# Optimization experiments

Hardware: AMD Instinct MI355X
Metric: run time of the kernel (lower is better)

The kernel has to match this reference:

```python
import jax, jax.numpy as jnp
import numpy as np

N_NODES = 100000


def setup_inputs() -> dict:
    key = jax.random.key(0)
    k1, k2, k3, k4, k5 = jax.random.split(key, 5)
    h = jax.random.normal(k1, (N_NODES, 128), dtype=jnp.float32)
    norm = jax.random.uniform(k2, (N_NODES, 1), dtype=jnp.float32)  # D^{-1/2}-style per-node norm
    W = jax.random.normal(k3, (128, 64), dtype=jnp.float32) * 0.05
    b = jnp.zeros((64,), dtype=jnp.float32)
    src = jax.random.randint(k4, (1600000,), 0, N_NODES, dtype=jnp.int32)
    dst = jax.random.randint(k5, (1600000,), 0, N_NODES, dtype=jnp.int32)
    return {"h": h, "norm": norm, "W": W, "b": b, "src": src, "dst": dst}


def reference(h, norm, W, b, src, dst):
    # Dense feature transform: g.ndata['h'] = h @ W   (dropout is identity at inference)
    hw = jnp.matmul(h, W)  # [N, out]
    # Message: src feature scaled by src norm
    msg = hw[src] * norm[src]  # [E, out]
    # Reduce: sum messages into dst, scale by dst norm
    agg = jax.ops.segment_sum(msg, dst, num_segments=N_NODES) * norm  # [N, out]
    out = agg + b
    return jax.nn.relu(out)
```

## Files before the change

kernel.cpp:

```cpp
#include <hip/hip_runtime.h>


typedef unsigned int u32;
typedef unsigned short u16;
typedef __attribute__((ext_vector_type(8))) short s16x8;
typedef __attribute__((ext_vector_type(4))) float f32x4;

#define NB_LOG 6
#define NPB 64
#define CAP 2048
#define MAXB 2048
#define EPB 8192
#define RT 256

__device__ __forceinline__ float bf2f(u16 v) {
  return __uint_as_float(((u32)v) << 16);
}
__device__ __forceinline__ u16 f2bf(float f) {
  u32 u = __float_as_uint(f);
  return (u16)((u + 0x7fffu + ((u >> 16) & 1u)) >> 16);
}
__device__ __forceinline__ void acc_bf16x4(float4& a, uint2 v) {
  a.x += __uint_as_float(v.x << 16);
  a.y += __uint_as_float(v.x & 0xFFFF0000u);
  a.z += __uint_as_float(v.y << 16);
  a.w += __uint_as_float(v.y & 0xFFFF0000u);
}

__global__ __launch_bounds__(256) void wconv(
    const float* __restrict__ W, u16* __restrict__ Wtg, u32* __restrict__ gcur) {
  int o = blockIdx.x * 256 + threadIdx.x;
  int j = o & 7, col = (o >> 3) & 15, kq = (o >> 7) & 3, ks = (o >> 9) & 3,
      ct = (o >> 11) & 3;
  int k = ks * 32 + kq * 8 + j;
  int n = ct * 16 + col;
  Wtg[o] = f2bf(W[k * 64 + n]);
  if (o < MAXB) gcur[o] = 0;
}

__global__ __launch_bounds__(256) void gemm_mfma(
    const float* __restrict__ h, const float* __restrict__ norm,
    const u16* __restrict__ Wtg, u16* __restrict__ scaledh, int N) {
  int lane = threadIdx.x & 63, wid = threadIdx.x >> 6;
  int col = lane & 15, kq = lane >> 4;

  s16x8 bfrag[4][4];
#pragma unroll
  for (int ct = 0; ct < 4; ++ct)
#pragma unroll
    for (int ks = 0; ks < 4; ++ks) {
      int f = ct * 16 + ks * 4 + kq;
      bfrag[ct][ks] =
          *reinterpret_cast<const s16x8*>(Wtg + ((size_t)(f * 16 + col) * 8));
    }

  int row0 = blockIdx.x * 64 + wid * 16;
  int myrow = row0 + col;
  int ldrow = myrow < N ? myrow : (N - 1);
  const float* __restrict__ hrow = h + (size_t)ldrow * 128 + kq * 8;

  f32x4 acc[4];
#pragma unroll
  for (int ct = 0; ct < 4; ++ct) acc[ct] = (f32x4){0.f, 0.f, 0.f, 0.f};

#pragma unroll
  for (int ks = 0; ks < 4; ++ks) {
    float4 x0 = *reinterpret_cast<const float4*>(hrow + ks * 32);
    float4 x1 = *reinterpret_cast<const float4*>(hrow + ks * 32 + 4);
    s16x8 a;
    a[0] = (short)f2bf(x0.x); a[1] = (short)f2bf(x0.y);
    a[2] = (short)f2bf(x0.z); a[3] = (short)f2bf(x0.w);
    a[4] = (short)f2bf(x1.x); a[5] = (short)f2bf(x1.y);
    a[6] = (short)f2bf(x1.z); a[7] = (short)f2bf(x1.w);
#pragma unroll
    for (int ct = 0; ct < 4; ++ct)
      acc[ct] =
          __builtin_amdgcn_mfma_f32_16x16x32_bf16(a, bfrag[ct][ks], acc[ct], 0, 0, 0);
  }

#pragma unroll
  for (int reg = 0; reg < 4; ++reg) {
    int node = row0 + kq * 4 + reg;
    if (node < N) {
      float nm = norm[node];
#pragma unroll
      for (int ct = 0; ct < 4; ++ct)
        scaledh[(size_t)node * 64 + ct * 16 + col] = f2bf(acc[ct][reg] * nm);
    }
  }
}

__global__ __launch_bounds__(1024) void bin_edges(
    const int* __restrict__ src, const int* __restrict__ dst,
    u32* __restrict__ gcur, u32* __restrict__ bins, int E) {
  __shared__ u32 lhist[MAXB];
  __shared__ u32 lbase[MAXB];
  int t = threadIdx.x;
  for (int i = t; i < MAXB; i += 1024) lhist[i] = 0;
  __syncthreads();
  int e0 = blockIdx.x * EPB;
  int s[8], d[8];
  u32 r[8];
#pragma unroll
  for (int k = 0; k < 8; ++k) {
    int e = e0 + k * 1024 + t;
    bool ok = e < E;
    s[k] = ok ? src[e] : 0;
    d[k] = ok ? dst[e] : -1;
  }
#pragma unroll
  for (int k = 0; k < 8; ++k) {
    if (d[k] >= 0) r[k] = atomicAdd(&lhist[d[k] >> NB_LOG], 1u);
  }
  __syncthreads();
  for (int i = t; i < MAXB; i += 1024) {
    u32 c = lhist[i];
    lbase[i] = c ? atomicAdd(&gcur[i], c) : 0u;
  }
  __syncthreads();
#pragma unroll
  for (int k = 0; k < 8; ++k) {
    if (d[k] >= 0) {
      int bk = d[k] >> NB_LOG;
      u32 p = lbase[bk] + r[k];
      if (p < CAP)
        bins[(size_t)bk * CAP + p] = ((u32)s[k] << NB_LOG) | (u32)(d[k] & (NPB - 1));
    }
  }
}

__global__ __launch_bounds__(RT) void bucket_reduce(
    const u16* __restrict__ scaledh, const u32* __restrict__ bins,
    const u32* __restrict__ gcur, const float* __restrict__ norm,
    const float4* __restrict__ bias4, float* __restrict__ out, int N) {
  __shared__ u32 hist[NPB];
  __shared__ u32 startp[NPB + 1];
  __shared__ u32 sorted[CAP];
  int bkt = blockIdx.x;
  int t = threadIdx.x, lane = t & 63, wid = t >> 6;
  int cnt = (int)gcur[bkt];
  if (cnt > CAP) cnt = CAP;
  if (t < NPB) hist[t] = 0;
  __syncthreads();

  const u32* __restrict__ my = bins + (size_t)bkt * CAP;
  u32 w[CAP / RT];
  u32 rk[CAP / RT];
#pragma unroll
  for (int k = 0; k < CAP / RT; ++k) {
    int e = k * RT + t;
    w[k] = (e < cnt) ? my[e] : 0xFFFFFFFFu;
  }
#pragma unroll
  for (int k = 0; k < CAP / RT; ++k) {
    if (w[k] != 0xFFFFFFFFu)
      rk[k] = atomicAdd(&hist[w[k] & (NPB - 1)], 1u);
  }
  __syncthreads();
  if (t < NPB) {
    u32 v = hist[t];
    u32 inc = v;
#pragma unroll
    for (int m = 1; m < NPB; m <<= 1) {
      u32 x = __shfl_up(inc, m);
      if (t >= m) inc += x;
    }
    startp[t] = inc - v;
    if (t == NPB - 1) startp[NPB] = inc;
  }
  __syncthreads();
#pragma unroll
  for (int k = 0; k < CAP / RT; ++k) {
    if (w[k] != 0xFFFFFFFFu)
      sorted[startp[w[k] & (NPB - 1)] + rk[k]] = w[k] >> NB_LOG;
  }
  __syncthreads();

  int grp = lane >> 4, c4 = lane & 15;
  float4 bl = bias4[c4];
  int base = bkt << NB_LOG;
  int cm1 = cnt - 1;
  const u16* __restrict__ sh = scaledh + (c4 << 2);
#pragma unroll
  for (int round = 0; round < 2; ++round) {
    int rA = (wid << 4) + (round << 3) + grp;
    int rB = rA + 4;
    int jA = (int)startp[rA], eA = (int)startp[rA + 1];
    int jB = (int)startp[rB], eB = (int)startp[rB + 1];
    float4 aA0 = make_float4(0.f, 0.f, 0.f, 0.f);
    float4 aA1 = make_float4(0.f, 0.f, 0.f, 0.f);
    float4 aB0 = make_float4(0.f, 0.f, 0.f, 0.f);
    float4 aB1 = make_float4(0.f, 0.f, 0.f, 0.f);
    while (jA < eA || jB < eB) {
      int iA0 = (int)sorted[min(jA + 0, cm1)];
      int iA1 = (int)sorted[min(jA + 1, cm1)];
      int iA2 = (int)sorted[min(jA + 2, cm1)];
      int iA3 = (int)sorted[min(jA + 3, cm1)];
      int iB0 = (int)sorted[min(jB + 0, cm1)];
      int iB1 = (int)sorted[min(jB + 1, cm1)];
      int iB2 = (int)sorted[min(jB + 2, cm1)];
      int iB3 = (int)sorted[min(jB + 3, cm1)];
      uint2 vA0 = *reinterpret_cast<const uint2*>(sh + ((size_t)iA0 << 6));
      uint2 vA1 = *reinterpret_cast<const uint2*>(sh + ((size_t)iA1 << 6));
      uint2 vA2 = *reinterpret_cast<const uint2*>(sh + ((size_t)iA2 << 6));
      uint2 vA3 = *reinterpret_cast<const uint2*>(sh + ((size_t)iA3 << 6));
      uint2 vB0 = *reinterpret_cast<const uint2*>(sh + ((size_t)iB0 << 6));
      uint2 vB1 = *reinterpret_cast<const uint2*>(sh + ((size_t)iB1 << 6));
      uint2 vB2 = *reinterpret_cast<const uint2*>(sh + ((size_t)iB2 << 6));
      uint2 vB3 = *reinterpret_cast<const uint2*>(sh + ((size_t)iB3 << 6));
      uint2 z = make_uint2(0u, 0u);
      vA0 = (jA + 0 < eA) ? vA0 : z;
      vA1 = (jA + 1 < eA) ? vA1 : z;
      vA2 = (jA + 2 < eA) ? vA2 : z;
      vA3 = (jA + 3 < eA) ? vA3 : z;
      vB0 = (jB + 0 < eB) ? vB0 : z;
      vB1 = (jB + 1 < eB) ? vB1 : z;
      vB2 = (jB + 2 < eB) ? vB2 : z;
      vB3 = (jB + 3 < eB) ? vB3 : z;
      acc_bf16x4(aA0, vA0);
      acc_bf16x4(aA1, vA1);
      acc_bf16x4(aA0, vA2);
      acc_bf16x4(aA1, vA3);
      acc_bf16x4(aB0, vB0);
      acc_bf16x4(aB1, vB1);
      acc_bf16x4(aB0, vB2);
      acc_bf16x4(aB1, vB3);
      jA += 4;
      jB += 4;
    }
    int nodeA = base + rA, nodeB = base + rB;
    if (nodeA < N) {
      float nm = norm[nodeA];
      float4 o;
      o.x = fmaxf(fmaf(aA0.x + aA1.x, nm, bl.x), 0.f);
      o.y = fmaxf(fmaf(aA0.y + aA1.y, nm, bl.y), 0.f);
      o.z = fmaxf(fmaf(aA0.z + aA1.z, nm, bl.z), 0.f);
      o.w = fmaxf(fmaf(aA0.w + aA1.w, nm, bl.w), 0.f);
      *reinterpret_cast<float4*>(out + (size_t)nodeA * 64 + (c4 << 2)) = o;
    }
    if (nodeB < N) {
      float nm = norm[nodeB];
      float4 o;
      o.x = fmaxf(fmaf(aB0.x + aB1.x, nm, bl.x), 0.f);
      o.y = fmaxf(fmaf(aB0.y + aB1.y, nm, bl.y), 0.f);
      o.z = fmaxf(fmaf(aB0.z + aB1.z, nm, bl.z), 0.f);
      o.w = fmaxf(fmaf(aB0.w + aB1.w, nm, bl.w), 0.f);
      *reinterpret_cast<float4*>(out + (size_t)nodeB * 64 + (c4 << 2)) = o;
    }
  }
}

__global__ __launch_bounds__(256) void zero_out(float4* __restrict__ o4, size_t n4) {
  size_t tid = blockIdx.x * 256 + threadIdx.x;
  size_t stride = (size_t)gridDim.x * 256;
  for (size_t i = tid; i < n4; i += stride) o4[i] = make_float4(0.f, 0.f, 0.f, 0.f);
}

__global__ __launch_bounds__(256) void scatter_edges(
    const u16* __restrict__ scaledh, const int* __restrict__ src,
    const int* __restrict__ dst, float* __restrict__ agg, int E) {
  int lane = threadIdx.x & 63;
  int gwid = (blockIdx.x * 256 + threadIdx.x) >> 6;
  int nw = (gridDim.x * 256) >> 6;
  for (int e = gwid; e < E; e += nw) {
    int s = __builtin_amdgcn_readfirstlane(src[e]);
    int d = __builtin_amdgcn_readfirstlane(dst[e]);
    float v = bf2f(scaledh[(size_t)s * 64 + lane]);
    unsafeAtomicAdd(&agg[(size_t)d * 64 + lane], v);
  }
}

__global__ __launch_bounds__(256) void finalize(
    float4* __restrict__ out4, const float* __restrict__ norm,
    const float4* __restrict__ b4, int N) {
  size_t total4 = (size_t)N * 16;
  size_t tid = blockIdx.x * 256 + threadIdx.x;
  size_t stride = (size_t)gridDim.x * 256;
  for (size_t t = tid; t < total4; t += stride) {
    int i = (int)(t >> 4), q = (int)(t & 15);
    float4 v = out4[t];
    float nm = norm[i];
    float4 bb = b4[q];
    v.x = fmaxf(fmaf(v.x, nm, bb.x), 0.f);
    v.y = fmaxf(fmaf(v.y, nm, bb.y), 0.f);
    v.z = fmaxf(fmaf(v.z, nm, bb.z), 0.f);
    v.w = fmaxf(fmaf(v.w, nm, bb.w), 0.f);
    out4[t] = v;
  }
}

extern "C" void kernel_launch(void* const* d_in, const int* in_sizes, int n_in,
                              void* d_out, int out_size, void* d_ws, size_t ws_size,
                              hipStream_t stream) {
  const float* h    = (const float*)d_in[0];
  const float* norm = (const float*)d_in[1];
  const float* W    = (const float*)d_in[2];
  const float* b    = (const float*)d_in[3];
  const int*   src  = (const int*)d_in[4];
  const int*   dst  = (const int*)d_in[5];

  int N = in_sizes[1];
  int E = in_sizes[4];
  int nbuckets = (N + NPB - 1) >> NB_LOG;
  int nrb = (N + 63) >> 6;
  int nbinb = (E + EPB - 1) / EPB;

  char* ws = (char*)d_ws;
  size_t off = 0;
  u16* scaledh = (u16*)(ws + off); off += (((size_t)N * 64 * 2) + 255) & ~(size_t)255;
  u32* gcur    = (u32*)(ws + off); off += (MAXB * 4 + 255) & ~(size_t)255;
  u16* Wtg     = (u16*)(ws + off); off += (8192 * 2 + 255) & ~(size_t)255;
  u32* bins    = (u32*)(ws + off); off += (size_t)MAXB * CAP * 4;
  size_t needed = off;
  size_t needed_fb = (size_t)((char*)bins - ws);

  if (ws_size >= needed && nbuckets <= MAXB) {
    wconv<<<32, 256, 0, stream>>>(W, Wtg, gcur);
    gemm_mfma<<<nrb, 256, 0, stream>>>(h, norm, Wtg, scaledh, N);
    bin_edges<<<nbinb, 1024, 0, stream>>>(src, dst, gcur, bins, E);
    bucket_reduce<<<nbuckets, RT, 0, stream>>>(scaledh, bins, gcur, norm,
                                               (const float4*)b, (float*)d_out, N);
  } else if (ws_size >= needed_fb) {
    float* agg = (float*)d_out;
    wconv<<<32, 256, 0, stream>>>(W, Wtg, gcur);
    gemm_mfma<<<nrb, 256, 0, stream>>>(h, norm, Wtg, scaledh, N);
    zero_out<<<1024, 256, 0, stream>>>((float4*)agg, (size_t)N * 16);
    scatter_edges<<<2048, 256, 0, stream>>>(scaledh, src, dst, agg, E);
    finalize<<<1024, 256, 0, stream>>>((float4*)agg, norm, (const float4*)b, N);
  }
}
```

Baseline: 79.12 us.

## Merge edge binning and MFMA GEMM into one launch with role-split blocks

The separate gemm_mfma and bin_edges launches are merged into one kernel. The first nbinb blocks bin edges and the remaining blocks each run the bf16 MFMA transform on 256 rows, using 16 waves of 1024 threads. The two independent stages can now run concurrently on the GPU, and one launch and its inter-kernel gap are removed. In exchange, GEMM blocks reserve the 16KB of shared memory the binning path needs and run at 1024 threads, which may lower occupancy. The original GEMM kernel is kept unchanged as a fallback variant.

```diff
diff --git a/kernel.cpp b/kernel.cpp
--- a/kernel.cpp
+++ b/kernel.cpp
@@ -12,6 +12,7 @@
 #define MAXB 2048
 #define EPB 8192
 #define RT 256
+#define GROWS 256
 
 __device__ __forceinline__ float bf2f(u16 v) {
   return __uint_as_float(((u32)v) << 16);
@@ -38,9 +39,50 @@
   if (o < MAXB) gcur[o] = 0;
 }
 
-__global__ __launch_bounds__(256) void gemm_mfma(
+__global__ __launch_bounds__(1024) void bin_and_gemm(
     const float* __restrict__ h, const float* __restrict__ norm,
-    const u16* __restrict__ Wtg, u16* __restrict__ scaledh, int N) {
+    const u16* __restrict__ Wtg, u16* __restrict__ scaledh, int N, int nbinb,
+    const int* __restrict__ src, const int* __restrict__ dst,
+    u32* __restrict__ gcur, u32* __restrict__ bins, int E) {
+  __shared__ u32 lhist[MAXB];
+  __shared__ u32 lbase[MAXB];
+
+  if ((int)blockIdx.x < nbinb) {
+    int t = threadIdx.x;
+    for (int i = t; i < MAXB; i += 1024) lhist[i] = 0;
+    __syncthreads();
+    int e0 = blockIdx.x * EPB;
+    int s[8], d[8];
+    u32 r[8];
+#pragma unroll
+    for (int k = 0; k < 8; ++k) {
+      int e = e0 + k * 1024 + t;
+      bool ok = e < E;
+      s[k] = ok ? src[e] : 0;
+      d[k] = ok ? dst[e] : -1;
+    }
+#pragma unroll
+    for (int k = 0; k < 8; ++k) {
+      if (d[k] >= 0) r[k] = atomicAdd(&lhist[d[k] >> NB_LOG], 1u);
+    }
+    __syncthreads();
+    for (int i = t; i < MAXB; i += 1024) {
+      u32 c = lhist[i];
+      lbase[i] = c ? atomicAdd(&gcur[i], c) : 0u;
+    }
+    __syncthreads();
+#pragma unroll
+    for (int k = 0; k < 8; ++k) {
+      if (d[k] >= 0) {
+        int bk = d[k] >> NB_LOG;
+        u32 p = lbase[bk] + r[k];
+        if (p < CAP)
+          bins[(size_t)bk * CAP + p] = ((u32)s[k] << NB_LOG) | (u32)(d[k] & (NPB - 1));
+      }
+    }
+    return;
+  }
+
   int lane = threadIdx.x & 63, wid = threadIdx.x >> 6;
   int col = lane & 15, kq = lane >> 4;
 
@@ -54,7 +96,7 @@
           *reinterpret_cast<const s16x8*>(Wtg + ((size_t)(f * 16 + col) * 8));
     }
 
-  int row0 = blockIdx.x * 64 + wid * 16;
+  int row0 = ((int)blockIdx.x - nbinb) * GROWS + wid * 16;
   int myrow = row0 + col;
   int ldrow = myrow < N ? myrow : (N - 1);
   const float* __restrict__ hrow = h + (size_t)ldrow * 128 + kq * 8;
@@ -86,45 +128,6 @@
 #pragma unroll
       for (int ct = 0; ct < 4; ++ct)
         scaledh[(size_t)node * 64 + ct * 16 + col] = f2bf(acc[ct][reg] * nm);
-    }
-  }
-}
-
-__global__ __launch_bounds__(1024) void bin_edges(
-    const int* __restrict__ src, const int* __restrict__ dst,
-    u32* __restrict__ gcur, u32* __restrict__ bins, int E) {
-  __shared__ u32 lhist[MAXB];
-  __shared__ u32 lbase[MAXB];
-  int t = threadIdx.x;
-  for (int i = t; i < MAXB; i += 1024) lhist[i] = 0;
-  __syncthreads();
-  int e0 = blockIdx.x * EPB;
-  int s[8], d[8];
-  u32 r[8];
-#pragma unroll
-  for (int k = 0; k < 8; ++k) {
-    int e = e0 + k * 1024 + t;
-    bool ok = e < E;
-    s[k] = ok ? src[e] : 0;
-    d[k] = ok ? dst[e] : -1;
-  }
-#pragma unroll
-  for (int k = 0; k < 8; ++k) {
-    if (d[k] >= 0) r[k] = atomicAdd(&lhist[d[k] >> NB_LOG], 1u);
-  }
-  __syncthreads();
-  for (int i = t; i < MAXB; i += 1024) {
-    u32 c = lhist[i];
-    lbase[i] = c ? atomicAdd(&gcur[i], c) : 0u;
-  }
-  __syncthreads();
-#pragma unroll
-  for (int k = 0; k < 8; ++k) {
-    if (d[k] >= 0) {
-      int bk = d[k] >> NB_LOG;
-      u32 p = lbase[bk] + r[k];
-      if (p < CAP)
-        bins[(size_t)bk * CAP + p] = ((u32)s[k] << NB_LOG) | (u32)(d[k] & (NPB - 1));
     }
   }
 }
@@ -250,6 +253,53 @@
   }
 }
 
+__global__ __launch_bounds__(256) void gemm_mfma_fb(
+    const float* __restrict__ h, const float* __restrict__ norm,
+    const u16* __restrict__ Wtg, u16* __restrict__ scaledh, int N) {
+  int lane = threadIdx.x & 63, wid = threadIdx.x >> 6;
+  int col = lane & 15, kq = lane >> 4;
+  s16x8 bfrag[4][4];
+#pragma unroll
+  for (int ct = 0; ct < 4; ++ct)
+#pragma unroll
+    for (int ks = 0; ks < 4; ++ks) {
+      int f = ct * 16 + ks * 4 + kq;
+      bfrag[ct][ks] =
+          *reinterpret_cast<const s16x8*>(Wtg + ((size_t)(f * 16 + col) * 8));
+    }
+  int row0 = blockIdx.x * 64 + wid * 16;
+  int myrow = row0 + col;
+  int ldrow = myrow < N ? myrow : (N - 1);
+  const float* __restrict__ hrow = h + (size_t)ldrow * 128 + kq * 8;
+  f32x4 acc[4];
+#pragma unroll
+  for (int ct = 0; ct < 4; ++ct) acc[ct] = (f32x4){0.f, 0.f, 0.f, 0.f};
+#pragma unroll
+  for (int ks = 0; ks < 4; ++ks) {
+    float4 x0 = *reinterpret_cast<const float4*>(hrow + ks * 32);
+    float4 x1 = *reinterpret_cast<const float4*>(hrow + ks * 32 + 4);
+    s16x8 a;
+    a[0] = (short)f2bf(x0.x); a[1] = (short)f2bf(x0.y);
+    a[2] = (short)f2bf(x0.z); a[3] = (short)f2bf(x0.w);
+    a[4] = (short)f2bf(x1.x); a[5] = (short)f2bf(x1.y);
+    a[6] = (short)f2bf(x1.z); a[7] = (short)f2bf(x1.w);
+#pragma unroll
+    for (int ct = 0; ct < 4; ++ct)
+      acc[ct] =
+          __builtin_amdgcn_mfma_f32_16x16x32_bf16(a, bfrag[ct][ks], acc[ct], 0, 0, 0);
+  }
+#pragma unroll
+  for (int reg = 0; reg < 4; ++reg) {
+    int node = row0 + kq * 4 + reg;
+    if (node < N) {
+      float nm = norm[node];
+#pragma unroll
+      for (int ct = 0; ct < 4; ++ct)
+        scaledh[(size_t)node * 64 + ct * 16 + col] = f2bf(acc[ct][reg] * nm);
+    }
+  }
+}
+
 __global__ __launch_bounds__(256) void zero_out(float4* __restrict__ o4, size_t n4) {
   size_t tid = blockIdx.x * 256 + threadIdx.x;
   size_t stride = (size_t)gridDim.x * 256;
@@ -302,7 +352,7 @@
   int N = in_sizes[1];
   int E = in_sizes[4];
   int nbuckets = (N + NPB - 1) >> NB_LOG;
-  int nrb = (N + 63) >> 6;
+  int ngb = (N + GROWS - 1) / GROWS;
   int nbinb = (E + EPB - 1) / EPB;
 
   char* ws = (char*)d_ws;
@@ -316,14 +366,14 @@
 
   if (ws_size >= needed && nbuckets <= MAXB) {
     wconv<<<32, 256, 0, stream>>>(W, Wtg, gcur);
-    gemm_mfma<<<nrb, 256, 0, stream>>>(h, norm, Wtg, scaledh, N);
-    bin_edges<<<nbinb, 1024, 0, stream>>>(src, dst, gcur, bins, E);
+    bin_and_gemm<<<nbinb + ngb, 1024, 0, stream>>>(h, norm, Wtg, scaledh, N, nbinb,
+                                                   src, dst, gcur, bins, E);
     bucket_reduce<<<nbuckets, RT, 0, stream>>>(scaledh, bins, gcur, norm,
                                                (const float4*)b, (float*)d_out, N);
   } else if (ws_size >= needed_fb) {
     float* agg = (float*)d_out;
     wconv<<<32, 256, 0, stream>>>(W, Wtg, gcur);
-    gemm_mfma<<<nrb, 256, 0, stream>>>(h, norm, Wtg, scaledh, N);
+    gemm_mfma_fb<<<(N + 63) >> 6, 256, 0, stream>>>(h, norm, Wtg, scaledh, N);
     zero_out<<<1024, 256, 0, stream>>>((float4*)agg, (size_t)N * 16);
     scatter_edges<<<2048, 256, 0, stream>>>(scaledh, src, dst, agg, E);
     finalize<<<1024, 256, 0, stream>>>((float4*)agg, norm, (const float4*)b, N);
```

Result: no change. 78.32 us (-1.0%).

## Slice feature columns into four planes and split bucket reduce into sort plus sliced gather

Applied to the files above, without the earlier changes.

The transformed features are now stored column-sliced (four planes of 16 bf16 columns per node). The fused bucket reduce is split into a sort kernel that writes sorted sources and per-bucket offsets back to global memory, and a slice_reduce launched with four blocks per bucket, each gathering one 32-byte slice per edge. The aim is more parallelism and a smaller per-slice gather working set that may fit better in cache. The cost is an extra kernel launch, writing and rereading the sorted bins, and narrower 4-byte gathers. The edge-binning kernel also now processes twice as many edges per block.

```diff
diff --git a/kernel.cpp b/kernel.cpp
--- a/kernel.cpp
+++ b/kernel.cpp
@@ -10,7 +10,7 @@
 #define NPB 64
 #define CAP 2048
 #define MAXB 2048
-#define EPB 8192
+#define EPB 16384
 #define RT 256
 
 __device__ __forceinline__ float bf2f(u16 v) {
@@ -20,11 +20,9 @@
   u32 u = __float_as_uint(f);
   return (u16)((u + 0x7fffu + ((u >> 16) & 1u)) >> 16);
 }
-__device__ __forceinline__ void acc_bf16x4(float4& a, uint2 v) {
-  a.x += __uint_as_float(v.x << 16);
-  a.y += __uint_as_float(v.x & 0xFFFF0000u);
-  a.z += __uint_as_float(v.y << 16);
-  a.w += __uint_as_float(v.y & 0xFFFF0000u);
+__device__ __forceinline__ void acc_bf16x2(float2& a, u32 v) {
+  a.x += __uint_as_float(v << 16);
+  a.y += __uint_as_float(v & 0xFFFF0000u);
 }
 
 __global__ __launch_bounds__(256) void wconv(
@@ -85,7 +83,8 @@
       float nm = norm[node];
 #pragma unroll
       for (int ct = 0; ct < 4; ++ct)
-        scaledh[(size_t)node * 64 + ct * 16 + col] = f2bf(acc[ct][reg] * nm);
+        scaledh[(size_t)ct * N * 16 + (size_t)node * 16 + col] =
+            f2bf(acc[ct][reg] * nm);
     }
   }
 }
@@ -99,17 +98,17 @@
   for (int i = t; i < MAXB; i += 1024) lhist[i] = 0;
   __syncthreads();
   int e0 = blockIdx.x * EPB;
-  int s[8], d[8];
-  u32 r[8];
-#pragma unroll
-  for (int k = 0; k < 8; ++k) {
+  int s[16], d[16];
+  u32 r[16];
+#pragma unroll
+  for (int k = 0; k < 16; ++k) {
     int e = e0 + k * 1024 + t;
     bool ok = e < E;
     s[k] = ok ? src[e] : 0;
     d[k] = ok ? dst[e] : -1;
   }
 #pragma unroll
-  for (int k = 0; k < 8; ++k) {
+  for (int k = 0; k < 16; ++k) {
     if (d[k] >= 0) r[k] = atomicAdd(&lhist[d[k] >> NB_LOG], 1u);
   }
   __syncthreads();
@@ -119,7 +118,7 @@
   }
   __syncthreads();
 #pragma unroll
-  for (int k = 0; k < 8; ++k) {
+  for (int k = 0; k < 16; ++k) {
     if (d[k] >= 0) {
       int bk = d[k] >> NB_LOG;
       u32 p = lbase[bk] + r[k];
@@ -129,21 +128,20 @@
   }
 }
 
-__global__ __launch_bounds__(RT) void bucket_reduce(
-    const u16* __restrict__ scaledh, const u32* __restrict__ bins,
-    const u32* __restrict__ gcur, const float* __restrict__ norm,
-    const float4* __restrict__ bias4, float* __restrict__ out, int N) {
+__global__ __launch_bounds__(RT) void sort_buckets(
+    u32* __restrict__ bins, const u32* __restrict__ gcur,
+    u32* __restrict__ gstart) {
   __shared__ u32 hist[NPB];
   __shared__ u32 startp[NPB + 1];
   __shared__ u32 sorted[CAP];
   int bkt = blockIdx.x;
-  int t = threadIdx.x, lane = t & 63, wid = t >> 6;
+  int t = threadIdx.x;
   int cnt = (int)gcur[bkt];
   if (cnt > CAP) cnt = CAP;
   if (t < NPB) hist[t] = 0;
   __syncthreads();
 
-  const u32* __restrict__ my = bins + (size_t)bkt * CAP;
+  u32* __restrict__ my = bins + (size_t)bkt * CAP;
   u32 w[CAP / RT];
   u32 rk[CAP / RT];
 #pragma unroll
@@ -175,78 +173,88 @@
       sorted[startp[w[k] & (NPB - 1)] + rk[k]] = w[k] >> NB_LOG;
   }
   __syncthreads();
-
-  int grp = lane >> 4, c4 = lane & 15;
-  float4 bl = bias4[c4];
+  for (int e = t; e < cnt; e += RT) my[e] = sorted[e];
+  if (t <= NPB) gstart[bkt * (NPB + 1) + t] = startp[t];
+}
+
+__global__ __launch_bounds__(RT) void slice_reduce(
+    const u16* __restrict__ scaledh, const u32* __restrict__ bins,
+    const u32* __restrict__ gcur, const u32* __restrict__ gstart,
+    const float* __restrict__ norm, const float* __restrict__ bias,
+    float* __restrict__ out, int N) {
+  __shared__ u32 sorted[CAP];
+  __shared__ u32 sp[NPB + 1];
+  int bkt = blockIdx.x >> 2;
+  int slice = blockIdx.x & 3;
+  int t = threadIdx.x, lane = t & 63, wid = t >> 6;
+  int cnt = (int)gcur[bkt];
+  if (cnt > CAP) cnt = CAP;
+  for (int e = t; e < cnt; e += RT) sorted[e] = bins[(size_t)bkt * CAP + e];
+  if (t <= NPB) sp[t] = gstart[bkt * (NPB + 1) + t];
+  __syncthreads();
+
+  int grp = lane >> 3, c8 = lane & 7;
+  const u16* __restrict__ sh = scaledh + (size_t)slice * N * 16 + (c8 << 1);
+  float2 bl = *reinterpret_cast<const float2*>(bias + slice * 16 + (c8 << 1));
   int base = bkt << NB_LOG;
   int cm1 = cnt - 1;
-  const u16* __restrict__ sh = scaledh + (c4 << 2);
-#pragma unroll
-  for (int round = 0; round < 2; ++round) {
-    int rA = (wid << 4) + (round << 3) + grp;
-    int rB = rA + 4;
-    int jA = (int)startp[rA], eA = (int)startp[rA + 1];
-    int jB = (int)startp[rB], eB = (int)startp[rB + 1];
-    float4 aA0 = make_float4(0.f, 0.f, 0.f, 0.f);
-    float4 aA1 = make_float4(0.f, 0.f, 0.f, 0.f);
-    float4 aB0 = make_float4(0.f, 0.f, 0.f, 0.f);
-    float4 aB1 = make_float4(0.f, 0.f, 0.f, 0.f);
-    while (jA < eA || jB < eB) {
-      int iA0 = (int)sorted[min(jA + 0, cm1)];
-      int iA1 = (int)sorted[min(jA + 1, cm1)];
-      int iA2 = (int)sorted[min(jA + 2, cm1)];
-      int iA3 = (int)sorted[min(jA + 3, cm1)];
-      int iB0 = (int)sorted[min(jB + 0, cm1)];
-      int iB1 = (int)sorted[min(jB + 1, cm1)];
-      int iB2 = (int)sorted[min(jB + 2, cm1)];
-      int iB3 = (int)sorted[min(jB + 3, cm1)];
-      uint2 vA0 = *reinterpret_cast<const uint2*>(sh + ((size_t)iA0 << 6));
-      uint2 vA1 = *reinterpret_cast<const uint2*>(sh + ((size_t)iA1 << 6));
-      uint2 vA2 = *reinterpret_cast<const uint2*>(sh + ((size_t)iA2 << 6));
-      uint2 vA3 = *reinterpret_cast<const uint2*>(sh + ((size_t)iA3 << 6));
-      uint2 vB0 = *reinterpret_cast<const uint2*>(sh + ((size_t)iB0 << 6));
-      uint2 vB1 = *reinterpret_cast<const uint2*>(sh + ((size_t)iB1 << 6));
-      uint2 vB2 = *reinterpret_cast<const uint2*>(sh + ((size_t)iB2 << 6));
-      uint2 vB3 = *reinterpret_cast<const uint2*>(sh + ((size_t)iB3 << 6));
-      uint2 z = make_uint2(0u, 0u);
-      vA0 = (jA + 0 < eA) ? vA0 : z;
-      vA1 = (jA + 1 < eA) ? vA1 : z;
-      vA2 = (jA + 2 < eA) ? vA2 : z;
-      vA3 = (jA + 3 < eA) ? vA3 : z;
-      vB0 = (jB + 0 < eB) ? vB0 : z;
-      vB1 = (jB + 1 < eB) ? vB1 : z;
-      vB2 = (jB + 2 < eB) ? vB2 : z;
-      vB3 = (jB + 3 < eB) ? vB3 : z;
-      acc_bf16x4(aA0, vA0);
-      acc_bf16x4(aA1, vA1);
-      acc_bf16x4(aA0, vA2);
-      acc_bf16x4(aA1, vA3);
-      acc_bf16x4(aB0, vB0);
-      acc_bf16x4(aB1, vB1);
-      acc_bf16x4(aB0, vB2);
-      acc_bf16x4(aB1, vB3);
-      jA += 4;
-      jB += 4;
-    }
-    int nodeA = base + rA, nodeB = base + rB;
-    if (nodeA < N) {
-      float nm = norm[nodeA];
-      float4 o;
-      o.x = fmaxf(fmaf(aA0.x + aA1.x, nm, bl.x), 0.f);
-      o.y = fmaxf(fmaf(aA0.y + aA1.y, nm, bl.y), 0.f);
-      o.z = fmaxf(fmaf(aA0.z + aA1.z, nm, bl.z), 0.f);
-      o.w = fmaxf(fmaf(aA0.w + aA1.w, nm, bl.w), 0.f);
-      *reinterpret_cast<float4*>(out + (size_t)nodeA * 64 + (c4 << 2)) = o;
-    }
-    if (nodeB < N) {
-      float nm = norm[nodeB];
-      float4 o;
-      o.x = fmaxf(fmaf(aB0.x + aB1.x, nm, bl.x), 0.f);
-      o.y = fmaxf(fmaf(aB0.y + aB1.y, nm, bl.y), 0.f);
-      o.z = fmaxf(fmaf(aB0.z + aB1.z, nm, bl.z), 0.f);
-      o.w = fmaxf(fmaf(aB0.w + aB1.w, nm, bl.w), 0.f);
-      *reinterpret_cast<float4*>(out + (size_t)nodeB * 64 + (c4 << 2)) = o;
-    }
+
+  int rA = (wid << 4) + grp;
+  int rB = rA + 8;
+  int jA = (int)sp[rA], eA = (int)sp[rA + 1];
+  int jB = (int)sp[rB], eB = (int)sp[rB + 1];
+  float2 aA0 = {0.f, 0.f}, aA1 = {0.f, 0.f};
+  float2 aB0 = {0.f, 0.f}, aB1 = {0.f, 0.f};
+  while (jA < eA || jB < eB) {
+    int iA0 = (int)sorted[min(jA + 0, cm1)];
+    int iA1 = (int)sorted[min(jA + 1, cm1)];
+    int iA2 = (int)sorted[min(jA + 2, cm1)];
+    int iA3 = (int)sorted[min(jA + 3, cm1)];
+    int iB0 = (int)sorted[min(jB + 0, cm1)];
+    int iB1 = (int)sorted[min(jB + 1, cm1)];
+    int iB2 = (int)sorted[min(jB + 2, cm1)];
+    int iB3 = (int)sorted[min(jB + 3, cm1)];
+    u32 vA0 = *reinterpret_cast<const u32*>(sh + ((size_t)iA0 << 4));
+    u32 vA1 = *reinterpret_cast<const u32*>(sh + ((size_t)iA1 << 4));
+    u32 vA2 = *reinterpret_cast<const u32*>(sh + ((size_t)iA2 << 4));
+    u32 vA3 = *reinterpret_cast<const u32*>(sh + ((size_t)iA3 << 4));
+    u32 vB0 = *reinterpret_cast<const u32*>(sh + ((size_t)iB0 << 4));
+    u32 vB1 = *reinterpret_cast<const u32*>(sh + ((size_t)iB1 << 4));
+    u32 vB2 = *reinterpret_cast<const u32*>(sh + ((size_t)iB2 << 4));
+    u32 vB3 = *reinterpret_cast<const u32*>(sh + ((size_t)iB3 << 4));
+    vA0 = (jA + 0 < eA) ? vA0 : 0u;
+    vA1 = (jA + 1 < eA) ? vA1 : 0u;
+    vA2 = (jA + 2 < eA) ? vA2 : 0u;
+    vA3 = (jA + 3 < eA) ? vA3 : 0u;
+    vB0 = (jB + 0 < eB) ? vB0 : 0u;
+    vB1 = (jB + 1 < eB) ? vB1 : 0u;
+    vB2 = (jB + 2 < eB) ? vB2 : 0u;
+    vB3 = (jB + 3 < eB) ? vB3 : 0u;
+    acc_bf16x2(aA0, vA0);
+    acc_bf16x2(aA1, vA1);
+    acc_bf16x2(aA0, vA2);
+    acc_bf16x2(aA1, vA3);
+    acc_bf16x2(aB0, vB0);
+    acc_bf16x2(aB1, vB1);
+    acc_bf16x2(aB0, vB2);
+    acc_bf16x2(aB1, vB3);
+    jA += 4;
+    jB += 4;
+  }
+  int nodeA = base + rA, nodeB = base + rB;
+  if (nodeA < N) {
+    float nm = norm[nodeA];
+    float2 o;
+    o.x = fmaxf(fmaf(aA0.x + aA1.x, nm, bl.x), 0.f);
+    o.y = fmaxf(fmaf(aA0.y + aA1.y, nm, bl.y), 0.f);
+    *reinterpret_cast<float2*>(out + (size_t)nodeA * 64 + slice * 16 + (c8 << 1)) = o;
+  }
+  if (nodeB < N) {
+    float nm = norm[nodeB];
+    float2 o;
+    o.x = fmaxf(fmaf(aB0.x + aB1.x, nm, bl.x), 0.f);
+    o.y = fmaxf(fmaf(aB0.y + aB1.y, nm, bl.y), 0.f);
+    *reinterpret_cast<float2*>(out + (size_t)nodeB * 64 + slice * 16 + (c8 << 1)) = o;
   }
 }
 
@@ -258,14 +266,15 @@
 
 __global__ __launch_bounds__(256) void scatter_edges(
     const u16* __restrict__ scaledh, const int* __restrict__ src,
-    const int* __restrict__ dst, float* __restrict__ agg, int E) {
+    const int* __restrict__ dst, float* __restrict__ agg, int E, int N) {
   int lane = threadIdx.x & 63;
   int gwid = (blockIdx.x * 256 + threadIdx.x) >> 6;
   int nw = (gridDim.x * 256) >> 6;
+  size_t sliceoff = (size_t)(lane >> 4) * N * 16 + (lane & 15);
   for (int e = gwid; e < E; e += nw) {
     int s = __builtin_amdgcn_readfirstlane(src[e]);
     int d = __builtin_amdgcn_readfirstlane(dst[e]);
-    float v = bf2f(scaledh[(size_t)s * 64 + lane]);
+    float v = bf2f(scaledh[sliceoff + (size_t)s * 16]);
     unsafeAtomicAdd(&agg[(size_t)d * 64 + lane], v);
   }
 }
@@ -310,22 +319,24 @@
   u16* scaledh = (u16*)(ws + off); off += (((size_t)N * 64 * 2) + 255) & ~(size_t)255;
   u32* gcur    = (u32*)(ws + off); off += (MAXB * 4 + 255) & ~(size_t)255;
   u16* Wtg     = (u16*)(ws + off); off += (8192 * 2 + 255) & ~(size_t)255;
+  u32* gstart  = (u32*)(ws + off); off += ((size_t)MAXB * (NPB + 1) * 4 + 255) & ~(size_t)255;
   u32* bins    = (u32*)(ws + off); off += (size_t)MAXB * CAP * 4;
   size_t needed = off;
-  size_t needed_fb = (size_t)((char*)bins - ws);
+  size_t needed_fb = (size_t)((char*)gstart - ws);
 
   if (ws_size >= needed && nbuckets <= MAXB) {
     wconv<<<32, 256, 0, stream>>>(W, Wtg, gcur);
     gemm_mfma<<<nrb, 256, 0, stream>>>(h, norm, Wtg, scaledh, N);
     bin_edges<<<nbinb, 1024, 0, stream>>>(src, dst, gcur, bins, E);
-    bucket_reduce<<<nbuckets, RT, 0, stream>>>(scaledh, bins, gcur, norm,
-                                               (const float4*)b, (float*)d_out, N);
+    sort_buckets<<<nbuckets, RT, 0, stream>>>(bins, gcur, gstart);
+    slice_reduce<<<nbuckets * 4, RT, 0, stream>>>(scaledh, bins, gcur, gstart,
+                                                  norm, b, (float*)d_out, N);
   } else if (ws_size >= needed_fb) {
     float* agg = (float*)d_out;
     wconv<<<32, 256, 0, stream>>>(W, Wtg, gcur);
     gemm_mfma<<<nrb, 256, 0, stream>>>(h, norm, Wtg, scaledh, N);
     zero_out<<<1024, 256, 0, stream>>>((float4*)agg, (size_t)N * 16);
-    scatter_edges<<<2048, 256, 0, stream>>>(scaledh, src, dst, agg, E);
+    scatter_edges<<<2048, 256, 0, stream>>>(scaledh, src, dst, agg, E, N);
     finalize<<<1024, 256, 0, stream>>>((float4*)agg, norm, (const float4*)b, N);
   }
 }
```

New measurement: 95.56 us. 20.8% more time.
